# Kernel optimization log

Measured on AMD Instinct MI355X. Metric: run time of the kernel, lower is better.

Reference implementation:

```python
import jax, jax.numpy as jnp
import numpy as np

S = 2          # scale_int = ceil(scale)
K = 3          # kernel size
OUTC = 3       # num_out_ch
NUM_FEAT = 64


def conv3x3(x, w, b):
    y = jax.lax.conv_general_dilated(x, w, (1, 1), ((1, 1), (1, 1)),
                                     dimension_numbers=('NCHW', 'OIHW', 'NCHW'))
    return y + b[None, :, None, None]


def unfold3x3(x):
    # torch F.unfold(x, 3, padding=1): (N, C*9, H*W), order c*9 + ki*3 + kj
    N, C, H, W = x.shape
    xp = jnp.pad(x, ((0, 0), (0, 0), (1, 1), (1, 1)))
    patches = jnp.stack([xp[:, :, i:i + H, j:j + W]
                         for i in range(3) for j in range(3)], axis=2)  # (N,C,9,H,W)
    return patches.reshape(N, C * 9, H * W)


def setup_inputs() -> dict:
    key = jax.random.key(0)
    ks = jax.random.split(key, 12)
    b, t, c, h, w = 2, 4, 16, 64, 64
    H, W = S * h, S * w
    nf4 = 64 // 4  # 16
    d_w = K * K * NUM_FEAT * OUTC  # 1728
    return {
        'x0': jax.random.normal(ks[0], (b, NUM_FEAT, h, w), jnp.float32),
        'feature': jax.random.normal(ks[1], (b, t, c, h, w), jnp.float32),
        'pos_mat': jax.random.uniform(ks[2], (H, W, 3), jnp.float32),
        'mask': jnp.ones((b, OUTC, H, W), dtype=bool),
        'conv1_w': jax.random.normal(ks[3], (nf4, 64, 3, 3), jnp.float32) * 0.05,
        'conv1_b': jnp.zeros((nf4,), jnp.float32),
        'conv2_w': jax.random.normal(ks[4], (nf4, nf4, 3, 3), jnp.float32) * 0.05,
        'conv2_b': jnp.zeros((nf4,), jnp.float32),
        'f2w1_w': jax.random.normal(ks[5], (256, nf4 + 1), jnp.float32) * 0.05,
        'f2w1_b': jnp.zeros((256,), jnp.float32),
        'f2w2_w': jax.random.normal(ks[6], (d_w, 256), jnp.float32) * 0.05,
        'f2w2_b': jnp.zeros((d_w,), jnp.float32),
    }


def reference(x0, feature, pos_mat, mask, conv1_w, conv1_b, conv2_w, conv2_b,
              f2w1_w, f2w1_b, f2w2_w, f2w2_b):
    b, t, c, h, w = feature.shape
    H, W = S * h, S * w
    # with_gradBack=False -> feature.detach()
    feat = jax.lax.stop_gradient(feature).reshape(b, t * c, h, w)
    # repeat_x(..., upsample=True): nearest-neighbour upsample by S
    feat_up = jnp.repeat(jnp.repeat(feat, S, axis=2), S, axis=3)  # (b,64,H,W)
    f = jax.nn.relu(conv3x3(feat_up, conv1_w, conv1_b))
    f = conv3x3(f, conv2_w, conv2_b)                              # (b,16,H,W)
    pos0 = jnp.transpose(pos_mat, (2, 0, 1))[0:1]                 # (1,H,W)
    fm = jnp.concatenate([f, jnp.broadcast_to(pos0[None], (b, 1, H, W))], axis=1)
    fm = fm.reshape(b, -1, H * W).transpose(0, 2, 1)              # (b,HW,17)
    hdn = jax.nn.relu(fm @ f2w1_w.T + f2w1_b)
    weights = hdn @ f2w2_w.T + f2w2_b                             # (b,HW,1728)
    weights = weights.reshape(b, h, S, w, S, K * K * NUM_FEAT, OUTC)
    weights = jnp.transpose(weights, (0, 2, 4, 1, 3, 5, 6))
    weights = weights.reshape(b, S * S, h * w, K * K * NUM_FEAT, OUTC)
    # repeat_x(x0) tiles x0 S^2 times -> all S^2 col copies identical; compute once
    cols = unfold3x3(x0).transpose(0, 2, 1)                       # (b,hw,576)
    out = jnp.einsum('bpk,bspko->bspo', cols, weights)            # (b,S^2,hw,3)
    out = jnp.transpose(out, (0, 1, 3, 2)).reshape(b, S, S, OUTC, h, w)
    out = jnp.transpose(out, (0, 3, 4, 1, 5, 2)).reshape(b, OUTC, H, W)
    # integer scale -> mask all True -> masked_select + view is identity
    return out, weights
```

## Files before the change

### kernel.cpp

```cpp
#include <hip/hip_runtime.h>

#define THREADS 256

#define Bsz 2
#define HWp 16384
#define Ntot (Bsz*HWp)
#define HID 256
#define Mm 1728
#define FMC 17
#define W_OFF 98304

#define F1_OFF  16384
#define F1_SZ   (Bsz*16*HWp)
#define FM_OFF  (F1_OFF + F1_SZ)

typedef __attribute__((ext_vector_type(8))) short bf16x8;
typedef __attribute__((ext_vector_type(4))) float f32x4;

static __device__ __forceinline__ short f2bf(float x) {
    unsigned u = __builtin_bit_cast(unsigned, x);
    unsigned r = (u + 0x7fff + ((u >> 16) & 1)) >> 16;
    return (short)r;
}

__global__ __launch_bounds__(THREADS) void k1_conv1(const float* __restrict__ feat,
                                                    const float* __restrict__ w1,
                                                    const float* __restrict__ b1,
                                                    float* __restrict__ f1) {
    __shared__ float sW[4 * 64 * 4];
    int tid = threadIdx.x;
    int t = blockIdx.x * THREADS + tid;
    int c = t & 63, r = (t >> 6) & 63, oc = (t >> 12) & 15, bb = t >> 16;

    #pragma unroll
    for (int q = 0; q < 4; ++q) {
        int e = tid * 4 + q;
        int v = e & 1, u = (e >> 1) & 1, ic = (e >> 2) & 63, pp = (e >> 8) & 3;
        int pi = pp >> 1, pj = pp & 1;
        float s = 0.f;
        for (int ki = 0; ki < 3; ++ki) {
            bool okki = pi ? (u ? (ki == 2) : (ki <= 1)) : (u ? (ki >= 1) : (ki == 0));
            if (!okki) continue;
            for (int kj = 0; kj < 3; ++kj) {
                bool okkj = pj ? (v ? (kj == 2) : (kj <= 1)) : (v ? (kj >= 1) : (kj == 0));
                if (okkj) s += w1[((oc * 64 + ic) * 3 + ki) * 3 + kj];
            }
        }
        sW[(pp * 64 + ic) * 4 + u * 2 + v] = s;
    }
    __syncthreads();

    float bias = b1[oc];
    float acc00 = bias, acc01 = bias, acc10 = bias, acc11 = bias;

    float my0 = (r > 0) ? 1.f : 0.f, my2 = (r < 63) ? 1.f : 0.f;
    float mx0 = (c > 0) ? 1.f : 0.f, mx2 = (c < 63) ? 1.f : 0.f;
    float m00 = my0 * mx0, m01 = my0, m02 = my0 * mx2;
    float m10 = mx0,       m12 = mx2;
    float m20 = my2 * mx0, m21 = my2, m22 = my2 * mx2;
    int ro0 = (r > 0) ? -64 : 0, ro2 = (r < 63) ? 64 : 0;
    int co0 = (c > 0) ? -1 : 0,  co2 = (c < 63) ? 1 : 0;

    const float* fb = feat + bb * 64 * 4096 + r * 64 + c;
    for (int ic = 0; ic < 64; ++ic) {
        const float* p1 = fb + ic * 4096;
        const float* p0 = p1 + ro0;
        const float* p2 = p1 + ro2;
        float v00 = p0[co0] * m00, v01 = p0[0] * m01, v02 = p0[co2] * m02;
        float v10 = p1[co0] * m10, v11 = p1[0],       v12 = p1[co2] * m12;
        float v20 = p2[co0] * m20, v21 = p2[0] * m21, v22 = p2[co2] * m22;

        f32x4 w0 = *(const f32x4*)(sW + (0 * 64 + ic) * 4);
        f32x4 w1v = *(const f32x4*)(sW + (1 * 64 + ic) * 4);
        f32x4 w2v = *(const f32x4*)(sW + (2 * 64 + ic) * 4);
        f32x4 w3 = *(const f32x4*)(sW + (3 * 64 + ic) * 4);

        acc00 = fmaf(w0[0], v00, acc00); acc00 = fmaf(w0[1], v01, acc00);
        acc00 = fmaf(w0[2], v10, acc00); acc00 = fmaf(w0[3], v11, acc00);
        acc01 = fmaf(w1v[0], v01, acc01); acc01 = fmaf(w1v[1], v02, acc01);
        acc01 = fmaf(w1v[2], v11, acc01); acc01 = fmaf(w1v[3], v12, acc01);
        acc10 = fmaf(w2v[0], v10, acc10); acc10 = fmaf(w2v[1], v11, acc10);
        acc10 = fmaf(w2v[2], v20, acc10); acc10 = fmaf(w2v[3], v21, acc10);
        acc11 = fmaf(w3[0], v11, acc11); acc11 = fmaf(w3[1], v12, acc11);
        acc11 = fmaf(w3[2], v21, acc11); acc11 = fmaf(w3[3], v22, acc11);
    }

    float* fo = f1 + (bb * 16 + oc) * HWp + (2 * r) * 128 + 2 * c;
    float2 r0 = make_float2(fmaxf(acc00, 0.f), fmaxf(acc01, 0.f));
    float2 r1 = make_float2(fmaxf(acc10, 0.f), fmaxf(acc11, 0.f));
    *reinterpret_cast<float2*>(fo) = r0;
    *reinterpret_cast<float2*>(fo + 128) = r1;
}

__global__ __launch_bounds__(THREADS) void k2_conv2_fm(const float* __restrict__ f1,
                                                       const float* __restrict__ w2,
                                                       const float* __restrict__ b2,
                                                       const float* __restrict__ pos,
                                                       float* __restrict__ fm) {
    int t = blockIdx.x * THREADS + threadIdx.x;
    if (t >= Bsz * FMC * HWp) return;
    int J = t & 127, I = (t >> 7) & 127;
    int bc = t >> 14;
    int ch = bc % FMC, bb = bc / FMC;
    int n = bb * HWp + I * 128 + J;
    float val;
    if (ch == 16) {
        val = pos[(I * 128 + J) * 3];
    } else {
        float acc = b2[ch];
        for (int ic = 0; ic < 16; ++ic) {
            const float* fb = f1 + (bb * 16 + ic) * HWp;
            const float* wb = w2 + (ch * 16 + ic) * 9;
            for (int ki = 0; ki < 3; ++ki) {
                int y = I + ki - 1;
                if ((unsigned)y >= 128u) continue;
                const float* row = fb + y * 128;
                for (int kj = 0; kj < 3; ++kj) {
                    int x = J + kj - 1;
                    if ((unsigned)x >= 128u) continue;
                    acc = fmaf(row[x], wb[ki * 3 + kj], acc);
                }
            }
        }
        val = acc;
    }
    fm[n * FMC + ch] = val;
}

__global__ __launch_bounds__(THREADS) void k3_cvtB(const float* __restrict__ w2g,
                                                   short* __restrict__ wB2) {
    int t = blockIdx.x * THREADS + threadIdx.x;
    int i = t & 7, l = (t >> 3) & 63, ct = (t >> 9) & 3, s = (t >> 11) & 7, mc = t >> 14;
    int col = mc * 64 + ct * 16 + (l & 15);
    int k = s * 32 + (l >> 4) * 8 + i;
    wB2[t] = f2bf(w2g[col * HID + k]);
}

__global__ __launch_bounds__(THREADS, 2) void k4_gemm(const float* __restrict__ fm,
                                                      const float* __restrict__ w1g,
                                                      const float* __restrict__ b1g,
                                                      const short* __restrict__ wB2,
                                                      const float* __restrict__ b2g,
                                                      const float* __restrict__ x0g,
                                                      float* __restrict__ dout) {
    __shared__ short    sA[16384];
    __shared__ float    sFM[64 * 20];
    __shared__ int      sOB[64];
    __shared__ float    sX[6528];
    __shared__ unsigned sLUT[1728];
    __shared__ float    sOut[4 * 64 * 3];

    int tid = threadIdx.x;
    int n0 = blockIdx.x * 64;
    int bb = n0 >> 14, tt = n0 & 16383, I = tt >> 7, J0 = tt & 127;
    int i0 = I >> 1, jmin = J0 >> 1;

    for (int idx = tid; idx < 64 * FMC; idx += THREADS) {
        int r = idx / FMC, i2 = idx - r * FMC;
        sFM[r * 20 + i2] = fm[n0 * FMC + idx];
    }
    if (tid < 64) {
        int n = n0 + tid;
        int J = J0 + tid;
        int s = ((I & 1) << 1) | (J & 1);
        int p = ((I >> 1) << 6) | (J >> 1);
        sOB[tid] = W_OFF + ((bb * 4 + s) * 4096 + p) * Mm;
    }
    for (int m = tid; m < Mm; m += THREADS) {
        int k = m / 3;
        int ch = k / 9, rem = k - ch * 9;
        int ki = rem / 3, kj = rem - ki * 3;
        sLUT[m] = (unsigned)((ch * 3 + ki) * 34 + kj);
    }
    {
        const float* x0b = x0g + bb * 64 * 4096;
        for (int e = tid; e < 6528; e += THREADS) {
            int ch = e / 102, r2 = e - ch * 102;
            int ki = r2 / 34, jc = r2 - ki * 34;
            int y = i0 + ki - 1, x = jmin + jc - 1;
            float v = 0.f;
            if ((unsigned)y < 64u && (unsigned)x < 64u) v = x0b[(ch * 64 + y) * 64 + x];
            sX[e] = v;
        }
    }
    __syncthreads();

    {
        float wreg[FMC];
        #pragma unroll
        for (int i = 0; i < FMC; ++i) wreg[i] = w1g[tid * FMC + i];
        float bj = b1g[tid];
        int g = (tid >> 3) & 7;
        int base = (tid >> 3) * 512 + (tid & 7);
        for (int rr = 0; rr < 64; ++rr) {
            int r = (rr + g) & 63;
            const float* fr = sFM + r * 20;
            f32x4 x0 = *(const f32x4*)fr;
            f32x4 x1 = *(const f32x4*)(fr + 4);
            f32x4 x2 = *(const f32x4*)(fr + 8);
            f32x4 x3 = *(const f32x4*)(fr + 12);
            float s = fmaf(fr[16], wreg[16], bj);
            s = fmaf(x0[0], wreg[0], s);  s = fmaf(x0[1], wreg[1], s);
            s = fmaf(x0[2], wreg[2], s);  s = fmaf(x0[3], wreg[3], s);
            s = fmaf(x1[0], wreg[4], s);  s = fmaf(x1[1], wreg[5], s);
            s = fmaf(x1[2], wreg[6], s);  s = fmaf(x1[3], wreg[7], s);
            s = fmaf(x2[0], wreg[8], s);  s = fmaf(x2[1], wreg[9], s);
            s = fmaf(x2[2], wreg[10], s); s = fmaf(x2[3], wreg[11], s);
            s = fmaf(x3[0], wreg[12], s); s = fmaf(x3[1], wreg[13], s);
            s = fmaf(x3[2], wreg[14], s); s = fmaf(x3[3], wreg[15], s);
            sA[base + r * 8] = f2bf(fmaxf(s, 0.f));
        }
    }
    __syncthreads();

    int wid = tid >> 6, l = tid & 63;
    int lm = l & 15, lg = l >> 4;
    int lm3 = lm % 3;

    int rowbase[4][4];
    #pragma unroll
    for (int rt = 0; rt < 4; ++rt)
        #pragma unroll
        for (int r = 0; r < 4; ++r)
            rowbase[rt][r] = sOB[rt * 16 + lg * 4 + r];

    int jl0[4], jl1[4];
    #pragma unroll
    for (int rt = 0; rt < 4; ++rt) {
        jl0[rt] = rt * 8 + lg * 2;
        jl1[rt] = rt * 8 + lg * 2 + 1;
    }

    const short* aptr = sA + lg * 512 + lm * 8;

    float racc[4][4][3];
    #pragma unroll
    for (int rt = 0; rt < 4; ++rt)
        #pragma unroll
        for (int r = 0; r < 4; ++r) {
            racc[rt][r][0] = 0.f; racc[rt][r][1] = 0.f; racc[rt][r][2] = 0.f;
        }

    for (int mc = wid; mc < 27; mc += 4) {
        int m0 = mc * 64;
        f32x4 acc[4][4];
        #pragma unroll
        for (int ct = 0; ct < 4; ++ct) {
            float bias = b2g[m0 + ct * 16 + lm];
            #pragma unroll
            for (int rt = 0; rt < 4; ++rt)
                acc[rt][ct] = (f32x4){bias, bias, bias, bias};
        }
        const short* bbase = wB2 + (size_t)mc * 16384 + l * 8;
        #pragma unroll 2
        for (int s = 0; s < 8; ++s) {
            bf16x8 af[4], bfr[4];
            #pragma unroll
            for (int rt = 0; rt < 4; ++rt)
                af[rt] = *(const bf16x8*)(aptr + s * 2048 + rt * 128);
            #pragma unroll
            for (int ct = 0; ct < 4; ++ct)
                bfr[ct] = *(const bf16x8*)(bbase + (s * 4 + ct) * 512);
            #pragma unroll
            for (int rt = 0; rt < 4; ++rt)
                #pragma unroll
                for (int ct = 0; ct < 4; ++ct)
                    acc[rt][ct] = __builtin_amdgcn_mfma_f32_16x16x32_bf16(
                        af[rt], bfr[ct], acc[rt][ct], 0, 0, 0);
        }
        #pragma unroll
        for (int rt = 0; rt < 4; ++rt)
            #pragma unroll
            for (int ct = 0; ct < 4; ++ct) {
                int cb = m0 + ct * 16 + lm;
                #pragma unroll
                for (int r = 0; r < 4; ++r)
                    dout[rowbase[rt][r] + cb] = acc[rt][ct][r];
            }
        unsigned cidx[4];
        #pragma unroll
        for (int ct = 0; ct < 4; ++ct) cidx[ct] = sLUT[m0 + ct * 16 + lm];
#define ACCUM(QB)                                                              \
        _Pragma("unroll")                                                      \
        for (int ct = 0; ct < 4; ++ct) {                                       \
            _Pragma("unroll")                                                  \
            for (int rt = 0; rt < 4; ++rt) {                                   \
                float v0 = sX[cidx[ct] + jl0[rt]];                             \
                float v1 = sX[cidx[ct] + jl1[rt]];                             \
                racc[rt][0][((QB) + ct) % 3] = fmaf(acc[rt][ct][0], v0,        \
                                racc[rt][0][((QB) + ct) % 3]);                 \
                racc[rt][1][((QB) + ct) % 3] = fmaf(acc[rt][ct][1], v0,        \
                                racc[rt][1][((QB) + ct) % 3]);                 \
                racc[rt][2][((QB) + ct) % 3] = fmaf(acc[rt][ct][2], v1,        \
                                racc[rt][2][((QB) + ct) % 3]);                 \
                racc[rt][3][((QB) + ct) % 3] = fmaf(acc[rt][ct][3], v1,        \
                                racc[rt][3][((QB) + ct) % 3]);                 \
            }                                                                  \
        }
        switch (mc % 3) {
            case 0: ACCUM(0); break;
            case 1: ACCUM(1); break;
            default: ACCUM(2); break;
        }
#undef ACCUM
    }

    #pragma unroll
    for (int rt = 0; rt < 4; ++rt)
        #pragma unroll
        for (int r = 0; r < 4; ++r) {
            float q0 = racc[rt][r][0], q1 = racc[rt][r][1], q2 = racc[rt][r][2];
            float a0 = (lm3 == 0) ? q0 : ((lm3 == 1) ? q2 : q1);
            float a1 = (lm3 == 0) ? q1 : ((lm3 == 1) ? q0 : q2);
            float a2 = (lm3 == 0) ? q2 : ((lm3 == 1) ? q1 : q0);
            #pragma unroll
            for (int off = 8; off > 0; off >>= 1) {
                a0 += __shfl_xor(a0, off, 64);
                a1 += __shfl_xor(a1, off, 64);
                a2 += __shfl_xor(a2, off, 64);
            }
            if (lm == 0) {
                int pix = rt * 16 + lg * 4 + r;
                float* so = sOut + (wid * 64 + pix) * 3;
                so[0] = a0; so[1] = a1; so[2] = a2;
            }
        }
    __syncthreads();
    if (tid < 192) {
        float s = sOut[tid] + sOut[192 + tid] + sOut[384 + tid] + sOut[576 + tid];
        int pix = tid / 3, o = tid - 3 * pix;
        dout[bb * 3 * HWp + o * HWp + I * 128 + J0 + pix] = s;
    }
}

extern "C" void kernel_launch(void* const* d_in, const int* in_sizes, int n_in,
                              void* d_out, int out_size, void* d_ws, size_t ws_size,
                              hipStream_t stream) {
    const float* x0      = (const float*)d_in[0];
    const float* feature = (const float*)d_in[1];
    const float* pos     = (const float*)d_in[2];
    const float* w1      = (const float*)d_in[4];
    const float* b1      = (const float*)d_in[5];
    const float* w2      = (const float*)d_in[6];
    const float* b2      = (const float*)d_in[7];
    const float* f2w1_w  = (const float*)d_in[8];
    const float* f2w1_b  = (const float*)d_in[9];
    const float* f2w2_w  = (const float*)d_in[10];
    const float* f2w2_b  = (const float*)d_in[11];

    float* out = (float*)d_out;
    float* ws  = (float*)d_ws;
    float* f1  = ws + F1_OFF;
    float* fm  = ws + FM_OFF;
    short* wB2 = (short*)(ws + F1_OFF);

    k1_conv1<<<(Bsz * 16 * 64 * 64) / THREADS, THREADS, 0, stream>>>(feature, w1, b1, f1);
    k2_conv2_fm<<<(Bsz * FMC * HWp) / THREADS, THREADS, 0, stream>>>(f1, w2, b2, pos, fm);
    k3_cvtB<<<(Mm * HID) / THREADS, THREADS, 0, stream>>>(f2w2_w, wB2);
    k4_gemm<<<Ntot / 64, THREADS, 0, stream>>>(fm, f2w1_w, f2w1_b, wB2, f2w2_b, x0, out);
}
```

Measured before the change: 126.8 us.

## Swap MFMA operands so each lane holds four consecutive weight columns for vector stores

The MFMA operands are swapped so the accumulator's four registers per lane map to four consecutive output columns of one pixel rather than four pixels of one column. The 1.4M-element weights tensor can then be written with 16-byte nontemporal vector stores instead of scalar stores. The fused einsum epilogue is restructured to match: the per-lane accumulator state shrinks from 48 to 12 floats, the LUT is read as uint4, and the cross-lane reduction drops from four shuffle steps to two. This mainly targets store efficiency on the write-bound weights output and reduces register pressure, at the cost of a rewritten, more intricate index mapping.

```diff
diff --git a/kernel.cpp b/kernel.cpp
--- a/kernel.cpp
+++ b/kernel.cpp
@@ -147,7 +147,7 @@
     __shared__ float    sFM[64 * 20];
     __shared__ int      sOB[64];
     __shared__ float    sX[6528];
-    __shared__ unsigned sLUT[1728];
+    __shared__ unsigned sLUT[1792];
     __shared__ float    sOut[4 * 64 * 3];
 
     int tid = threadIdx.x;
@@ -160,7 +160,6 @@
         sFM[r * 20 + i2] = fm[n0 * FMC + idx];
     }
     if (tid < 64) {
-        int n = n0 + tid;
         int J = J0 + tid;
         int s = ((I & 1) << 1) | (J & 1);
         int p = ((I >> 1) << 6) | (J >> 1);
@@ -215,41 +214,32 @@
 
     int wid = tid >> 6, l = tid & 63;
     int lm = l & 15, lg = l >> 4;
-    int lm3 = lm % 3;
-
-    int rowbase[4][4];
-    #pragma unroll
-    for (int rt = 0; rt < 4; ++rt)
-        #pragma unroll
-        for (int r = 0; r < 4; ++r)
-            rowbase[rt][r] = sOB[rt * 16 + lg * 4 + r];
-
-    int jl0[4], jl1[4];
+    int lg3 = lg % 3;
+
+    int pixbase[4], jl[4];
     #pragma unroll
     for (int rt = 0; rt < 4; ++rt) {
-        jl0[rt] = rt * 8 + lg * 2;
-        jl1[rt] = rt * 8 + lg * 2 + 1;
+        pixbase[rt] = sOB[rt * 16 + lm];
+        jl[rt] = rt * 8 + (lm >> 1);
     }
 
     const short* aptr = sA + lg * 512 + lm * 8;
 
-    float racc[4][4][3];
+    float racc[4][3];
     #pragma unroll
-    for (int rt = 0; rt < 4; ++rt)
-        #pragma unroll
-        for (int r = 0; r < 4; ++r) {
-            racc[rt][r][0] = 0.f; racc[rt][r][1] = 0.f; racc[rt][r][2] = 0.f;
-        }
+    for (int rt = 0; rt < 4; ++rt) {
+        racc[rt][0] = 0.f; racc[rt][1] = 0.f; racc[rt][2] = 0.f;
+    }
 
     for (int mc = wid; mc < 27; mc += 4) {
         int m0 = mc * 64;
         f32x4 acc[4][4];
         #pragma unroll
         for (int ct = 0; ct < 4; ++ct) {
-            float bias = b2g[m0 + ct * 16 + lm];
+            f32x4 bias4 = *(const f32x4*)(b2g + m0 + ct * 16 + lg * 4);
             #pragma unroll
             for (int rt = 0; rt < 4; ++rt)
-                acc[rt][ct] = (f32x4){bias, bias, bias, bias};
+                acc[rt][ct] = bias4;
         }
         const short* bbase = wB2 + (size_t)mc * 16384 + l * 8;
         #pragma unroll 2
@@ -266,35 +256,27 @@
                 #pragma unroll
                 for (int ct = 0; ct < 4; ++ct)
                     acc[rt][ct] = __builtin_amdgcn_mfma_f32_16x16x32_bf16(
-                        af[rt], bfr[ct], acc[rt][ct], 0, 0, 0);
+                        bfr[ct], af[rt], acc[rt][ct], 0, 0, 0);
         }
         #pragma unroll
         for (int rt = 0; rt < 4; ++rt)
             #pragma unroll
-            for (int ct = 0; ct < 4; ++ct) {
-                int cb = m0 + ct * 16 + lm;
-                #pragma unroll
-                for (int r = 0; r < 4; ++r)
-                    dout[rowbase[rt][r] + cb] = acc[rt][ct][r];
-            }
-        unsigned cidx[4];
-        #pragma unroll
-        for (int ct = 0; ct < 4; ++ct) cidx[ct] = sLUT[m0 + ct * 16 + lm];
+            for (int ct = 0; ct < 4; ++ct)
+                __builtin_nontemporal_store(acc[rt][ct],
+                    (f32x4*)(dout + pixbase[rt] + m0 + ct * 16 + lg * 4));
+        unsigned lutv[4];
 #define ACCUM(QB)                                                              \
         _Pragma("unroll")                                                      \
         for (int ct = 0; ct < 4; ++ct) {                                       \
+            *(uint4*)lutv = *(const uint4*)(sLUT + m0 + ct * 16 + lg * 4);     \
             _Pragma("unroll")                                                  \
-            for (int rt = 0; rt < 4; ++rt) {                                   \
-                float v0 = sX[cidx[ct] + jl0[rt]];                             \
-                float v1 = sX[cidx[ct] + jl1[rt]];                             \
-                racc[rt][0][((QB) + ct) % 3] = fmaf(acc[rt][ct][0], v0,        \
-                                racc[rt][0][((QB) + ct) % 3]);                 \
-                racc[rt][1][((QB) + ct) % 3] = fmaf(acc[rt][ct][1], v0,        \
-                                racc[rt][1][((QB) + ct) % 3]);                 \
-                racc[rt][2][((QB) + ct) % 3] = fmaf(acc[rt][ct][2], v1,        \
-                                racc[rt][2][((QB) + ct) % 3]);                 \
-                racc[rt][3][((QB) + ct) % 3] = fmaf(acc[rt][ct][3], v1,        \
-                                racc[rt][3][((QB) + ct) % 3]);                 \
+            for (int r = 0; r < 4; ++r) {                                      \
+                _Pragma("unroll")                                              \
+                for (int rt = 0; rt < 4; ++rt) {                               \
+                    float v = sX[lutv[r] + jl[rt]];                            \
+                    racc[rt][((QB) + ct + r) % 3] =                            \
+                        fmaf(acc[rt][ct][r], v, racc[rt][((QB) + ct + r) % 3]);\
+                }                                                              \
             }                                                                  \
         }
         switch (mc % 3) {
@@ -306,30 +288,24 @@
     }
 
     #pragma unroll
-    for (int rt = 0; rt < 4; ++rt)
-        #pragma unroll
-        for (int r = 0; r < 4; ++r) {
-            float q0 = racc[rt][r][0], q1 = racc[rt][r][1], q2 = racc[rt][r][2];
-            float a0 = (lm3 == 0) ? q0 : ((lm3 == 1) ? q2 : q1);
-            float a1 = (lm3 == 0) ? q1 : ((lm3 == 1) ? q0 : q2);
-            float a2 = (lm3 == 0) ? q2 : ((lm3 == 1) ? q1 : q0);
-            #pragma unroll
-            for (int off = 8; off > 0; off >>= 1) {
-                a0 += __shfl_xor(a0, off, 64);
-                a1 += __shfl_xor(a1, off, 64);
-                a2 += __shfl_xor(a2, off, 64);
-            }
-            if (lm == 0) {
-                int pix = rt * 16 + lg * 4 + r;
-                float* so = sOut + (wid * 64 + pix) * 3;
-                so[0] = a0; so[1] = a1; so[2] = a2;
-            }
-        }
+    for (int rt = 0; rt < 4; ++rt) {
+        float q0 = racc[rt][0], q1 = racc[rt][1], q2 = racc[rt][2];
+        float a0 = (lg3 == 0) ? q0 : ((lg3 == 1) ? q2 : q1);
+        float a1 = (lg3 == 0) ? q1 : ((lg3 == 1) ? q0 : q2);
+        float a2 = (lg3 == 0) ? q2 : ((lg3 == 1) ? q1 : q0);
+        a0 += __shfl_xor(a0, 16, 64); a0 += __shfl_xor(a0, 32, 64);
+        a1 += __shfl_xor(a1, 16, 64); a1 += __shfl_xor(a1, 32, 64);
+        a2 += __shfl_xor(a2, 16, 64); a2 += __shfl_xor(a2, 32, 64);
+        if (l < 16) {
+            float* so = sOut + (wid * 64 + rt * 16 + lm) * 3;
+            so[0] = a0; so[1] = a1; so[2] = a2;
+        }
+    }
     __syncthreads();
     if (tid < 192) {
         float s = sOut[tid] + sOut[192 + tid] + sOut[384 + tid] + sOut[576 + tid];
         int pix = tid / 3, o = tid - 3 * pix;
-        dout[bb * 3 * HWp + o * HWp + I * 128 + J0 + pix] = s;
+        __builtin_nontemporal_store(s, dout + bb * 3 * HWp + o * HWp + I * 128 + J0 + pix);
     }
 }
 
```

Result: slower. 141.2 us (+11.4%).
